# Kernel optimization log

Hardware: AMD Instinct MI355X
Metric: run time of the kernel (lower is better)

The kernel has to match this reference:

```python
import jax, jax.numpy as jnp
import numpy as np

N = 50000        # nodes (users + candidates)
E = 1_600_000    # edges (interactions), avg degree 32
IN = 128         # in_channels
OUT = 128        # out_channels (GRU hidden)
HEAD = 16        # final linear head


def setup_inputs() -> dict:
    key = jax.random.key(0)
    ks = jax.random.split(key, 16)
    sx = 1.0 / np.sqrt(IN)
    sh = 1.0 / np.sqrt(OUT)
    return {
        "x": jax.random.normal(ks[0], (N, IN), jnp.float32),
        "edge_index": jax.random.randint(ks[1], (2, E), 0, N, dtype=jnp.int64),
        "edge_weight": jax.random.uniform(ks[2], (E,), jnp.float32),
        # graph-conv GRU gate weights (update z, reset r, candidate h)
        "W_xz": jax.random.normal(ks[3], (IN, OUT), jnp.float32) * sx,
        "W_hz": jax.random.normal(ks[4], (OUT, OUT), jnp.float32) * sh,
        "b_z": jnp.zeros((OUT,), jnp.float32),
        "W_xr": jax.random.normal(ks[5], (IN, OUT), jnp.float32) * sx,
        "W_hr": jax.random.normal(ks[6], (OUT, OUT), jnp.float32) * sh,
        "b_r": jnp.zeros((OUT,), jnp.float32),
        "W_xh": jax.random.normal(ks[7], (IN, OUT), jnp.float32) * sx,
        "W_hh": jax.random.normal(ks[8], (OUT, OUT), jnp.float32) * sh,
        "b_h": jnp.zeros((OUT,), jnp.float32),
        # final linear head: Linear(out_channels, 16)
        "W_lin": jax.random.normal(ks[9], (OUT, HEAD), jnp.float32) * sh,
        "b_lin": jnp.zeros((HEAD,), jnp.float32),
    }


def reference(x, edge_index, edge_weight,
              W_xz, W_hz, b_z, W_xr, W_hr, b_r, W_xh, W_hh, b_h,
              W_lin, b_lin):
    src, dst = edge_index[0], edge_index[1]

    # symmetric degree normalization from edge weights
    deg_out = jax.ops.segment_sum(edge_weight, src, num_segments=N)
    deg_in = jax.ops.segment_sum(edge_weight, dst, num_segments=N)
    inv_sqrt_out = jnp.where(deg_out > 0, 1.0 / jnp.sqrt(deg_out), 0.0)
    inv_sqrt_in = jnp.where(deg_in > 0, 1.0 / jnp.sqrt(deg_in), 0.0)
    norm = edge_weight * inv_sqrt_out[src] * inv_sqrt_in[dst]  # [E]

    def gconv(feat, W):
        # GCN-style conv: normalized weighted scatter-sum of transformed feats
        m = feat @ W                                   # [N, OUT]
        msg = m[src] * norm[:, None]                   # [E, OUT] gather
        return jax.ops.segment_sum(msg, dst, num_segments=N)  # scatter

    h = jnp.zeros((N, OUT), x.dtype)  # initial recurrent hidden state

    # GRU with graph-conv gates (GConvGRU-style recurrent cell)
    z = jax.nn.sigmoid(gconv(x, W_xz) + gconv(h, W_hz) + b_z)
    r = jax.nn.sigmoid(gconv(x, W_xr) + gconv(h, W_hr) + b_r)
    h_tilde = jnp.tanh(gconv(x, W_xh) + gconv(r * h, W_hh) + b_h)
    h_new = z * h + (1.0 - z) * h_tilde               # [N, OUT]

    return h_new @ W_lin + b_lin                       # [N, 16]
```

## Files before the change

### kernel.cpp

```cpp
#include <hip/hip_runtime.h>
#include <hip/hip_bf16.h>
#include <hip/hip_fp16.h>


#define CH 128
#define HEADS 16
#define TM 64
#define KC 32
#define DRANGE 12800
#define DSLICES 64
#define RN 98
#define NR 512
#define NB 256
#define SCAP 3840

typedef _Float16 half8 __attribute__((ext_vector_type(8)));
typedef _Float16 half4v __attribute__((ext_vector_type(4)));
typedef float floatx4 __attribute__((ext_vector_type(4)));

__global__ __launch_bounds__(256) void k_deg(const int* __restrict__ src,
                                             const float* __restrict__ w,
                                             float* __restrict__ partial, int E) {
    __shared__ float h[DRANGE];
    const int r = blockIdx.x / DSLICES;
    const int sl = blockIdx.x % DSLICES;
    const int base = r * DRANGE;
    for (int i = threadIdx.x; i < DRANGE; i += 256) h[i] = 0.f;
    __syncthreads();
    const int per = (E + DSLICES - 1) / DSLICES;
    const int lo = sl * per;
    const int hi = min(lo + per, E);
    int e = lo + threadIdx.x * 4;
    for (; e + 3 < hi; e += 1024) {
        int4 s4 = *reinterpret_cast<const int4*>(src + e);
        float4 w4 = *reinterpret_cast<const float4*>(w + e);
        int a;
        a = s4.x - base; if ((unsigned)a < DRANGE) atomicAdd(&h[a], w4.x);
        a = s4.y - base; if ((unsigned)a < DRANGE) atomicAdd(&h[a], w4.y);
        a = s4.z - base; if ((unsigned)a < DRANGE) atomicAdd(&h[a], w4.z);
        a = s4.w - base; if ((unsigned)a < DRANGE) atomicAdd(&h[a], w4.w);
    }
    for (; e < hi; ++e) {
        int a = src[e] - base;
        if ((unsigned)a < DRANGE) atomicAdd(&h[a], w[e]);
    }
    __syncthreads();
    float* dstp = partial + ((size_t)r * DSLICES + sl) * DRANGE;
    for (int i = threadIdx.x; i < DRANGE; i += 256) dstp[i] = h[i];
}

__global__ __launch_bounds__(256) void k_degxcw(const float* __restrict__ partial,
                                                const float* __restrict__ x,
                                                __half* __restrict__ xh,
                                                const float* __restrict__ Wxz,
                                                const float* __restrict__ Wxh,
                                                const float* __restrict__ Wlin,
                                                __half* __restrict__ WzT,
                                                __half* __restrict__ WhT,
                                                __half* __restrict__ WlT,
                                                int n, int nbdeg) {
    const int t = threadIdx.x;
    if ((int)blockIdx.x >= nbdeg) {
        int i = (blockIdx.x - nbdeg) * 256 + t;
        if (i < CH * CH) {
            int nn = i >> 7, k = i & 127;
            WzT[i] = __float2half(Wxz[k * CH + nn]);
            WhT[i] = __float2half(Wxh[k * CH + nn]);
        } else if (i < CH * CH + HEADS * CH) {
            int j = i - CH * CH;
            int nn = j >> 7, k = j & 127;
            WlT[j] = __float2half(Wlin[k * HEADS + nn]);
        }
        return;
    }
    __shared__ float degl[256];
    const int bb = blockIdx.x * 256;
    int i = bb + t;
    if (i < n) {
        int r = i / DRANGE;
        int idx = i - r * DRANGE;
        const float* p = partial + (size_t)r * DSLICES * DRANGE + idx;
        float s = 0.f;
#pragma unroll 8
        for (int sl = 0; sl < DSLICES; ++sl) s += p[(size_t)sl * DRANGE];
        degl[t] = s;
    }
    __syncthreads();
#pragma unroll
    for (int g = 0; g < 16; ++g) {
        int ln = g * 16 + (t >> 4);
        int node = bb + ln;
        if (node >= n) break;
        int c8 = (t & 15) * 8;
        float dg = degl[ln];
        float sc = dg > 0.f ? rsqrtf(dg) : 0.f;
        float4 a = *reinterpret_cast<const float4*>(x + (size_t)node * CH + c8);
        float4 b = *reinterpret_cast<const float4*>(x + (size_t)node * CH + c8 + 4);
        __half2 h0 = __floats2half2_rn(a.x * sc, a.y * sc);
        __half2 h1 = __floats2half2_rn(a.z * sc, a.w * sc);
        __half2 h2 = __floats2half2_rn(b.x * sc, b.y * sc);
        __half2 h3 = __floats2half2_rn(b.z * sc, b.w * sc);
        uint4 packed = make_uint4(*(unsigned*)&h0, *(unsigned*)&h1, *(unsigned*)&h2, *(unsigned*)&h3);
        *reinterpret_cast<uint4*>(xh + (size_t)node * CH + c8) = packed;
    }
}

__global__ __launch_bounds__(256) void k_count(const int* __restrict__ dst,
                                               unsigned* __restrict__ counts, int E) {
    __shared__ unsigned h[NR];
    const int b = blockIdx.x;
    for (int i = threadIdx.x; i < NR; i += 256) h[i] = 0u;
    __syncthreads();
    const int per = (E + NB - 1) / NB;
    const int lo = b * per;
    const int hi = min(lo + per, E);
    for (int e = lo + threadIdx.x; e < hi; e += 256)
        atomicAdd(&h[dst[e] / RN], 1u);
    __syncthreads();
    for (int i = threadIdx.x; i < NR; i += 256) counts[(size_t)i * NB + b] = h[i];
}

__global__ __launch_bounds__(256) void k_scanR(unsigned* __restrict__ counts,
                                               unsigned* __restrict__ total) {
    __shared__ unsigned s[256];
    const int r = blockIdx.x;
    const int t = threadIdx.x;
    unsigned v = counts[(size_t)r * NB + t];
    s[t] = v;
    __syncthreads();
    for (int ofs = 1; ofs < 256; ofs <<= 1) {
        unsigned u = (t >= ofs) ? s[t - ofs] : 0u;
        __syncthreads();
        s[t] += u;
        __syncthreads();
    }
    counts[(size_t)r * NB + t] = s[t] - v;
    if (t == 255) total[r] = s[255];
}

__global__ __launch_bounds__(256) void k_part(const int* __restrict__ src,
                                              const int* __restrict__ dst,
                                              const float* __restrict__ w,
                                              const unsigned* __restrict__ counts,
                                              const unsigned* __restrict__ total,
                                              int2* __restrict__ rec2, int E) {
    __shared__ unsigned cursor[NR];
    __shared__ unsigned sa[NR], sb[NR];
    const int b = blockIdx.x;
    const int t = threadIdx.x;
    sa[t] = total[t]; sa[t + 256] = total[t + 256];
    __syncthreads();
    unsigned* cur = sa; unsigned* nxt = sb;
    for (int ofs = 1; ofs < NR; ofs <<= 1) {
        for (int k = t; k < NR; k += 256) {
            unsigned v = cur[k];
            if (k >= ofs) v += cur[k - ofs];
            nxt[k] = v;
        }
        __syncthreads();
        unsigned* tmp = cur; cur = nxt; nxt = tmp;
    }
    for (int r = t; r < NR; r += 256) {
        unsigned rb = cur[r] - total[r];
        cursor[r] = rb + counts[(size_t)r * NB + b];
    }
    __syncthreads();
    const int per = (E + NB - 1) / NB;
    const int lo = b * per;
    const int hi = min(lo + per, E);
    for (int e = lo + t; e < hi; e += 256) {
        int d = dst[e];
        int r = d / RN;
        int dl = d - r * RN;
        unsigned pos = atomicAdd(&cursor[r], 1u);
        rec2[pos] = make_int2(__float_as_int(w[e]), (dl << 16) | src[e]);
    }
}

__global__ __launch_bounds__(1024) void k_sortgather(const unsigned* __restrict__ total,
                                                     const int2* __restrict__ rec2,
                                                     unsigned* __restrict__ rec3,
                                                     const __half* __restrict__ xh,
                                                     __half* __restrict__ xaggh, int n) {
    __shared__ int2 stage[SCAP];
    __shared__ unsigned sortedP[SCAP];
    __shared__ unsigned hist[RN], curx[RN];
    __shared__ unsigned sa[NR], sb[NR];
    const int r = blockIdx.x;
    const int bn = r * RN;
    if (bn >= n) return;
    const int rn = min(RN, n - bn);
    const int t = threadIdx.x;

    if (t < NR) sa[t] = total[t];
    __syncthreads();
    unsigned* cur = sa; unsigned* nxt = sb;
    for (int ofs = 1; ofs < NR; ofs <<= 1) {
        if (t < NR) {
            unsigned v = cur[t];
            if (t >= ofs) v += cur[t - ofs];
            nxt[t] = v;
        }
        __syncthreads();
        unsigned* tmp = cur; cur = nxt; nxt = tmp;
    }
    const unsigned tot = total[r];
    const unsigned gbase = cur[r] - tot;

    if (t < RN) hist[t] = 0u;
    __syncthreads();
    for (unsigned i = t; i < tot; i += 1024) {
        int2 v = rec2[gbase + i];
        if (i < SCAP) stage[i] = v;
        atomicAdd(&hist[v.y >> 16], 1u);
    }
    __syncthreads();
    if (t == 0) {
        unsigned run = 0;
        for (int j = 0; j < rn; ++j) {
            unsigned c = hist[j];
            hist[j] = run;
            curx[j] = run;
            run += c;
        }
    }
    __syncthreads();
    const bool big = (tot > SCAP);
    for (unsigned i = t; i < tot; i += 1024) {
        int2 v = (i < SCAP) ? stage[i] : rec2[gbase + i];
        int dl = v.y >> 16;
        __half hw = __float2half(__int_as_float(v.x));
        unsigned packed = ((unsigned)__half_as_ushort(hw) << 16) | (unsigned)(v.y & 0xFFFF);
        unsigned pos = atomicAdd(&curx[dl], 1u);
        if (big) rec3[gbase + pos] = packed;
        else sortedP[pos] = packed;
    }
    __syncthreads();

    const int hwid = t >> 5;
    const int lane = t & 31;
    const __half* xb = xh + lane * 4;
    const unsigned* grec = rec3 + gbase;
    for (int nd = hwid; nd < rn; nd += 32) {
        unsigned i = hist[nd];
        unsigned end = curx[nd];
        float acc0 = 0.f, acc1 = 0.f, acc2 = 0.f, acc3 = 0.f;
        float wsum = 0.f;
        for (; i + 8 <= end; i += 8) {
            unsigned r0, r1, r2, r3, r4, r5, r6, r7;
            if (big) {
                r0 = grec[i];     r1 = grec[i + 1]; r2 = grec[i + 2]; r3 = grec[i + 3];
                r4 = grec[i + 4]; r5 = grec[i + 5]; r6 = grec[i + 6]; r7 = grec[i + 7];
            } else {
                r0 = sortedP[i];     r1 = sortedP[i + 1]; r2 = sortedP[i + 2]; r3 = sortedP[i + 3];
                r4 = sortedP[i + 4]; r5 = sortedP[i + 5]; r6 = sortedP[i + 6]; r7 = sortedP[i + 7];
            }
            half4v v0 = *reinterpret_cast<const half4v*>(xb + (size_t)(r0 & 0xFFFFu) * CH);
            half4v v1 = *reinterpret_cast<const half4v*>(xb + (size_t)(r1 & 0xFFFFu) * CH);
            half4v v2 = *reinterpret_cast<const half4v*>(xb + (size_t)(r2 & 0xFFFFu) * CH);
            half4v v3 = *reinterpret_cast<const half4v*>(xb + (size_t)(r3 & 0xFFFFu) * CH);
            half4v v4 = *reinterpret_cast<const half4v*>(xb + (size_t)(r4 & 0xFFFFu) * CH);
            half4v v5 = *reinterpret_cast<const half4v*>(xb + (size_t)(r5 & 0xFFFFu) * CH);
            half4v v6 = *reinterpret_cast<const half4v*>(xb + (size_t)(r6 & 0xFFFFu) * CH);
            half4v v7 = *reinterpret_cast<const half4v*>(xb + (size_t)(r7 & 0xFFFFu) * CH);
            float w0 = __half2float(__ushort_as_half((unsigned short)(r0 >> 16)));
            float w1 = __half2float(__ushort_as_half((unsigned short)(r1 >> 16)));
            float w2 = __half2float(__ushort_as_half((unsigned short)(r2 >> 16)));
            float w3 = __half2float(__ushort_as_half((unsigned short)(r3 >> 16)));
            float w4 = __half2float(__ushort_as_half((unsigned short)(r4 >> 16)));
            float w5 = __half2float(__ushort_as_half((unsigned short)(r5 >> 16)));
            float w6 = __half2float(__ushort_as_half((unsigned short)(r6 >> 16)));
            float w7 = __half2float(__ushort_as_half((unsigned short)(r7 >> 16)));
            wsum += ((w0 + w1) + (w2 + w3)) + ((w4 + w5) + (w6 + w7));
            acc0 = fmaf(w0, (float)v0[0], acc0); acc1 = fmaf(w0, (float)v0[1], acc1);
            acc2 = fmaf(w0, (float)v0[2], acc2); acc3 = fmaf(w0, (float)v0[3], acc3);
            acc0 = fmaf(w1, (float)v1[0], acc0); acc1 = fmaf(w1, (float)v1[1], acc1);
            acc2 = fmaf(w1, (float)v1[2], acc2); acc3 = fmaf(w1, (float)v1[3], acc3);
            acc0 = fmaf(w2, (float)v2[0], acc0); acc1 = fmaf(w2, (float)v2[1], acc1);
            acc2 = fmaf(w2, (float)v2[2], acc2); acc3 = fmaf(w2, (float)v2[3], acc3);
            acc0 = fmaf(w3, (float)v3[0], acc0); acc1 = fmaf(w3, (float)v3[1], acc1);
            acc2 = fmaf(w3, (float)v3[2], acc2); acc3 = fmaf(w3, (float)v3[3], acc3);
            acc0 = fmaf(w4, (float)v4[0], acc0); acc1 = fmaf(w4, (float)v4[1], acc1);
            acc2 = fmaf(w4, (float)v4[2], acc2); acc3 = fmaf(w4, (float)v4[3], acc3);
            acc0 = fmaf(w5, (float)v5[0], acc0); acc1 = fmaf(w5, (float)v5[1], acc1);
            acc2 = fmaf(w5, (float)v5[2], acc2); acc3 = fmaf(w5, (float)v5[3], acc3);
            acc0 = fmaf(w6, (float)v6[0], acc0); acc1 = fmaf(w6, (float)v6[1], acc1);
            acc2 = fmaf(w6, (float)v6[2], acc2); acc3 = fmaf(w6, (float)v6[3], acc3);
            acc0 = fmaf(w7, (float)v7[0], acc0); acc1 = fmaf(w7, (float)v7[1], acc1);
            acc2 = fmaf(w7, (float)v7[2], acc2); acc3 = fmaf(w7, (float)v7[3], acc3);
        }
        for (; i < end; ++i) {
            unsigned r0 = big ? grec[i] : sortedP[i];
            float w0 = __half2float(__ushort_as_half((unsigned short)(r0 >> 16)));
            half4v v0 = *reinterpret_cast<const half4v*>(xb + (size_t)(r0 & 0xFFFFu) * CH);
            wsum += w0;
            acc0 = fmaf(w0, (float)v0[0], acc0); acc1 = fmaf(w0, (float)v0[1], acc1);
            acc2 = fmaf(w0, (float)v0[2], acc2); acc3 = fmaf(w0, (float)v0[3], acc3);
        }
        float sc = wsum > 0.f ? rsqrtf(wsum) : 0.f;
        half4v hv;
        hv[0] = (_Float16)(acc0 * sc); hv[1] = (_Float16)(acc1 * sc);
        hv[2] = (_Float16)(acc2 * sc); hv[3] = (_Float16)(acc3 * sc);
        *reinterpret_cast<half4v*>(xaggh + (size_t)(bn + nd) * CH + lane * 4) = hv;
    }
}

__global__ __launch_bounds__(256) void k_final3(const __half* __restrict__ xaggh,
                                                const __half* __restrict__ WzT,
                                                const __half* __restrict__ WhT,
                                                const __half* __restrict__ WlT,
                                                const float* __restrict__ bz,
                                                const float* __restrict__ bh,
                                                const float* __restrict__ blin,
                                                float* __restrict__ out, int n) {
    __shared__ __half gL[4][16][136];
    const int tid = threadIdx.x;
    const int w = tid >> 6;
    const int l = tid & 63;
    const int lr = l & 15;
    const int lk = l >> 4;
    const int nodeb = blockIdx.x * 64 + w * 16;

    int arow = nodeb + lr;
    if (arow > n - 1) arow = n - 1;

    floatx4 accz[8], acch[8];
#pragma unroll
    for (int ct = 0; ct < 8; ++ct) {
        accz[ct] = (floatx4){0.f, 0.f, 0.f, 0.f};
        acch[ct] = (floatx4){0.f, 0.f, 0.f, 0.f};
    }

#pragma unroll
    for (int kc = 0; kc < 4; ++kc) {
        half8 a = *reinterpret_cast<const half8*>(xaggh + (size_t)arow * CH + kc * 32 + lk * 8);
#pragma unroll
        for (int ct = 0; ct < 8; ++ct) {
            half8 bzf = *reinterpret_cast<const half8*>(WzT + (ct * 16 + lr) * CH + kc * 32 + lk * 8);
            accz[ct] = __builtin_amdgcn_mfma_f32_16x16x32_f16(a, bzf, accz[ct], 0, 0, 0);
            half8 bhf = *reinterpret_cast<const half8*>(WhT + (ct * 16 + lr) * CH + kc * 32 + lk * 8);
            acch[ct] = __builtin_amdgcn_mfma_f32_16x16x32_f16(a, bhf, acch[ct], 0, 0, 0);
        }
    }

#pragma unroll
    for (int ct = 0; ct < 8; ++ct) {
        float bzv = bz[ct * 16 + lr];
        float bhv = bh[ct * 16 + lr];
#pragma unroll
        for (int r = 0; r < 4; ++r) {
            float zp = accz[ct][r] + bzv;
            float hp = acch[ct][r] + bhv;
            float g = (1.f - 1.f / (1.f + __expf(-zp))) * tanhf(hp);
            gL[w][lk * 4 + r][ct * 16 + lr] = __float2half(g);
        }
    }
    __syncthreads();

    floatx4 acco = (floatx4){0.f, 0.f, 0.f, 0.f};
#pragma unroll
    for (int kc = 0; kc < 4; ++kc) {
        half8 a = *reinterpret_cast<const half8*>(&gL[w][lr][kc * 32 + lk * 8]);
        half8 b = *reinterpret_cast<const half8*>(WlT + lr * CH + kc * 32 + lk * 8);
        acco = __builtin_amdgcn_mfma_f32_16x16x32_f16(a, b, acco, 0, 0, 0);
    }
    float bl = blin[lr];
#pragma unroll
    for (int r = 0; r < 4; ++r) {
        int node = nodeb + lk * 4 + r;
        if (node < n) out[(size_t)node * HEADS + lr] = acco[r] + bl;
    }
}

__global__ __launch_bounds__(256) void k1B(const int* __restrict__ src,
                                           const int* __restrict__ dst,
                                           const float* __restrict__ w,
                                           float* __restrict__ deg_out,
                                           unsigned* __restrict__ cnt, int E) {
    int e = blockIdx.x * blockDim.x + threadIdx.x;
    if (e >= E) return;
    unsafeAtomicAdd(deg_out + src[e], w[e]);
    atomicAdd(cnt + dst[e], 1u);
}

__global__ __launch_bounds__(1024) void k_scan(unsigned* __restrict__ off, int n) {
    __shared__ unsigned s[1024];
    const int t = threadIdx.x;
    const int per = (n + 1023) / 1024;
    int lo = t * per;
    int hi = lo + per; if (hi > n) hi = n;
    unsigned sum = 0;
    for (int i = lo; i < hi; ++i) sum += off[i];
    s[t] = sum;
    __syncthreads();
    for (int ofs = 1; ofs < 1024; ofs <<= 1) {
        unsigned v = (t >= ofs) ? s[t - ofs] : 0u;
        __syncthreads();
        s[t] += v;
        __syncthreads();
    }
    unsigned run = s[t] - sum;
    for (int i = lo; i < hi; ++i) {
        unsigned c = off[i];
        off[i] = run;
        run += c;
    }
}

__global__ __launch_bounds__(256) void k_fillB(const int* __restrict__ src,
                                               const int* __restrict__ dst,
                                               const float* __restrict__ w,
                                               unsigned* __restrict__ off,
                                               int2* __restrict__ rec, int E) {
    int e = blockIdx.x * blockDim.x + threadIdx.x;
    if (e >= E) return;
    unsigned pos = atomicAdd(off + dst[e], 1u);
    rec[pos] = make_int2(__float_as_int(w[e]), src[e]);
}

__global__ __launch_bounds__(256) void k_gatherB(const unsigned* __restrict__ off,
                                                 const int2* __restrict__ rec,
                                                 const float* __restrict__ deg_out,
                                                 const float* __restrict__ x,
                                                 float* __restrict__ xagg, int n) {
    int node = blockIdx.x * 4 + (threadIdx.x >> 6);
    if (node >= n) return;
    int lane = threadIdx.x & 63;
    unsigned i = node ? off[node - 1] : 0u;
    unsigned end = off[node];
    float2 acc = make_float2(0.f, 0.f);
    float wsum = 0.f;
    for (; i < end; ++i) {
        int2 r0 = rec[i];
        float w0 = __int_as_float(r0.x);
        float d0 = deg_out[r0.y];
        float c0 = w0 * (d0 > 0.f ? rsqrtf(d0) : 0.f);
        float2 v = *reinterpret_cast<const float2*>(x + (size_t)r0.y * CH + lane * 2);
        wsum += w0;
        acc.x = fmaf(c0, v.x, acc.x);
        acc.y = fmaf(c0, v.y, acc.y);
    }
    float sc = wsum > 0.f ? rsqrtf(wsum) : 0.f;
    *reinterpret_cast<float2*>(xagg + (size_t)node * CH + lane * 2) =
        make_float2(acc.x * sc, acc.y * sc);
}

__global__ __launch_bounds__(256) void k_final2(const float* __restrict__ xagg,
                                                const float* __restrict__ Wxz,
                                                const float* __restrict__ bz,
                                                const float* __restrict__ Wxh,
                                                const float* __restrict__ bh,
                                                const float* __restrict__ Wlin,
                                                const float* __restrict__ blin,
                                                float* __restrict__ out, int n) {
    __shared__ float smem[10560];
    float* sA = smem;
    float* sWz = smem + 2304;
    float* sWh = smem + 6400;

    const int tid = threadIdx.x;
    const int tx = tid & 31;
    const int ty = tid >> 5;
    const int base = blockIdx.x * TM;

    float az[8][4] = {{0.f}};
    float ah[8][4] = {{0.f}};

    for (int kc = 0; kc < CH; kc += KC) {
        {
            int i = tid;
#pragma unroll
            for (int r2 = 0; r2 < 2; ++r2, i += 256) {
                int row = i >> 3;
                int c4 = (i & 7) * 4;
                int grow = base + row; if (grow > n - 1) grow = n - 1;
                float4 v = *reinterpret_cast<const float4*>(xagg + (size_t)grow * CH + kc + c4);
                *reinterpret_cast<float4*>(&sA[row * 36 + c4]) = v;
            }
            int j = tid;
#pragma unroll
            for (int r2 = 0; r2 < 4; ++r2, j += 256) {
                int row = j >> 5;
                int c4 = (j & 31) * 4;
                *reinterpret_cast<float4*>(&sWz[row * 128 + c4]) =
                    *reinterpret_cast<const float4*>(Wxz + (size_t)(kc + row) * CH + c4);
                *reinterpret_cast<float4*>(&sWh[row * 128 + c4]) =
                    *reinterpret_cast<const float4*>(Wxh + (size_t)(kc + row) * CH + c4);
            }
        }
        __syncthreads();
#pragma unroll 4
        for (int kk = 0; kk < KC; ++kk) {
            float4 wz = *reinterpret_cast<float4*>(&sWz[kk * 128 + tx * 4]);
            float4 wh = *reinterpret_cast<float4*>(&sWh[kk * 128 + tx * 4]);
#pragma unroll
            for (int r = 0; r < 8; ++r) {
                float a = sA[(ty * 8 + r) * 36 + kk];
                az[r][0] = fmaf(a, wz.x, az[r][0]);
                az[r][1] = fmaf(a, wz.y, az[r][1]);
                az[r][2] = fmaf(a, wz.z, az[r][2]);
                az[r][3] = fmaf(a, wz.w, az[r][3]);
                ah[r][0] = fmaf(a, wh.x, ah[r][0]);
                ah[r][1] = fmaf(a, wh.y, ah[r][1]);
                ah[r][2] = fmaf(a, wh.z, ah[r][2]);
                ah[r][3] = fmaf(a, wh.w, ah[r][3]);
            }
        }
        __syncthreads();
    }

    float* sG = smem;
    const float4 bz4 = *reinterpret_cast<const float4*>(bz + tx * 4);
    const float4 bh4 = *reinterpret_cast<const float4*>(bh + tx * 4);
#pragma unroll
    for (int r = 0; r < 8; ++r) {
        int row = ty * 8 + r;
        float4 g4;
        float zp = az[r][0] + bz4.x, hp = ah[r][0] + bh4.x;
        g4.x = (1.f - 1.f / (1.f + __expf(-zp))) * tanhf(hp);
        zp = az[r][1] + bz4.y; hp = ah[r][1] + bh4.y;
        g4.y = (1.f - 1.f / (1.f + __expf(-zp))) * tanhf(hp);
        zp = az[r][2] + bz4.z; hp = ah[r][2] + bh4.z;
        g4.z = (1.f - 1.f / (1.f + __expf(-zp))) * tanhf(hp);
        zp = az[r][3] + bz4.w; hp = ah[r][3] + bh4.w;
        g4.w = (1.f - 1.f / (1.f + __expf(-zp))) * tanhf(hp);
        *reinterpret_cast<float4*>(&sG[row * 132 + tx * 4]) = g4;
    }
    __syncthreads();

#pragma unroll
    for (int it = 0; it < 4; ++it) {
        int idx = it * 256 + tid;
        int node = idx >> 4;
        int hh = idx & 15;
        float acc = blin[hh];
#pragma unroll 8
        for (int j = 0; j < CH; ++j)
            acc = fmaf(sG[node * 132 + j], Wlin[j * HEADS + hh], acc);
        if (base + node < n) out[(size_t)(base + node) * HEADS + hh] = acc;
    }
}

static inline size_t align256(size_t v) { return (v + 255) & ~(size_t)255; }

extern "C" void kernel_launch(void* const* d_in, const int* in_sizes, int n_in,
                              void* d_out, int out_size, void* d_ws, size_t ws_size,
                              hipStream_t stream) {
    const float* x = (const float*)d_in[0];
    const int* ei = (const int*)d_in[1];
    const float* w = (const float*)d_in[2];
    const float* Wxz = (const float*)d_in[3];
    const float* bz = (const float*)d_in[5];
    const float* Wxh = (const float*)d_in[9];
    const float* bh = (const float*)d_in[11];
    const float* Wlin = (const float*)d_in[12];
    const float* blin = (const float*)d_in[13];
    float* out = (float*)d_out;

    const int Nn = in_sizes[0] / CH;
    const int E = in_sizes[2];

    const int* src = ei;
    const int* dst = ei + E;
    int eb = (E + 255) / 256;
    char* base = (char*)d_ws;

    size_t off_counts = 0;
    size_t off_total = align256(off_counts + (size_t)NR * NB * 4);
    size_t off_xh = align256(off_total + NR * 4);
    size_t off_xaggh = align256(off_xh + (size_t)Nn * CH * 2);
    size_t off_wz = align256(off_xaggh + (size_t)Nn * CH * 2);
    size_t off_wh = align256(off_wz + (size_t)CH * CH * 2);
    size_t off_wl = align256(off_wh + (size_t)CH * CH * 2);
    size_t off_rec2 = align256(off_wl + (size_t)HEADS * CH * 2);
    size_t off_rec3 = align256(off_rec2 + (size_t)E * 8);
    size_t needNew = off_rec3 + (size_t)E * 4;
    size_t partial_bytes = (size_t)4 * DSLICES * DRANGE * 4;

    if (ws_size >= needNew && Nn <= 65536 && (size_t)NR * RN >= (size_t)Nn &&
        partial_bytes <= (size_t)E * 12) {
        unsigned* counts = (unsigned*)(base + off_counts);
        unsigned* total = (unsigned*)(base + off_total);
        __half* xh = (__half*)(base + off_xh);
        __half* xaggh = (__half*)(base + off_xaggh);
        __half* WzT = (__half*)(base + off_wz);
        __half* WhT = (__half*)(base + off_wh);
        __half* WlT = (__half*)(base + off_wl);
        int2* rec2 = (int2*)(base + off_rec2);
        unsigned* rec3 = (unsigned*)(base + off_rec3);
        float* partial = (float*)(base + off_rec2);

        int nbdeg = (Nn + 255) / 256;
        int nbw = (CH * CH + HEADS * CH + 255) / 256;

        k_deg<<<4 * DSLICES, 256, 0, stream>>>(src, w, partial, E);
        k_degxcw<<<nbdeg + nbw, 256, 0, stream>>>(partial, x, xh, Wxz, Wxh, Wlin,
                                                  WzT, WhT, WlT, Nn, nbdeg);
        k_count<<<NB, 256, 0, stream>>>(dst, counts, E);
        k_scanR<<<NR, 256, 0, stream>>>(counts, total);
        k_part<<<NB, 256, 0, stream>>>(src, dst, w, counts, total, rec2, E);
        k_sortgather<<<NR, 1024, 0, stream>>>(total, rec2, rec3, xh, xaggh, Nn);
        k_final3<<<(Nn + 63) / 64, 256, 0, stream>>>(xaggh, WzT, WhT, WlT, bz, bh, blin, out, Nn);
    } else {
        unsigned* off = (unsigned*)base;
        float* deg_out = (float*)(base + (size_t)Nn * 4);
        int2* rec = (int2*)(base + (size_t)2 * Nn * 4);
        float* xagg = (float*)((char*)rec + (size_t)E * 8);

        hipMemsetAsync(d_ws, 0, (size_t)2 * Nn * 4, stream);
        k1B<<<eb, 256, 0, stream>>>(src, dst, w, deg_out, off, E);
        k_scan<<<1, 1024, 0, stream>>>(off, Nn);
        k_fillB<<<eb, 256, 0, stream>>>(src, dst, w, off, rec, E);
        k_gatherB<<<(Nn + 3) / 4, 256, 0, stream>>>(off, rec, deg_out, x, xagg, Nn);
        k_final2<<<(Nn + TM - 1) / TM, 256, 0, stream>>>(xagg, Wxz, bz, Wxh, bh, Wlin, blin, out, Nn);
    }
}
```

Measured before the change: 160.2 us.

## Halve destination bucket size, use 512-thread sort-gather blocks, fuse count into prep kernel

Halves the destination range per bucket (98→49 nodes, 512→1024 buckets) and runs the sort-gather kernel with 512 threads per block, shrinking its shared staging area. The goal is more and lighter blocks, better occupancy and load balance in the gather. The dst-histogram count kernel is merged into the degree/convert kernel as extra blocks, removing one launch. In exchange the prefix scans cover twice as many buckets and more buckets overflow to global memory because of the smaller staging capacity.

```diff
diff --git a/kernel.cpp b/kernel.cpp
--- a/kernel.cpp
+++ b/kernel.cpp
@@ -9,10 +9,10 @@
 #define KC 32
 #define DRANGE 12800
 #define DSLICES 64
-#define RN 98
-#define NR 512
+#define RN 49
+#define NR 1024
 #define NB 256
-#define SCAP 3840
+#define SCAP 2048
 
 typedef _Float16 half8 __attribute__((ext_vector_type(8)));
 typedef _Float16 half4v __attribute__((ext_vector_type(4)));
@@ -49,19 +49,36 @@
     for (int i = threadIdx.x; i < DRANGE; i += 256) dstp[i] = h[i];
 }
 
-__global__ __launch_bounds__(256) void k_degxcw(const float* __restrict__ partial,
-                                                const float* __restrict__ x,
-                                                __half* __restrict__ xh,
-                                                const float* __restrict__ Wxz,
-                                                const float* __restrict__ Wxh,
-                                                const float* __restrict__ Wlin,
-                                                __half* __restrict__ WzT,
-                                                __half* __restrict__ WhT,
-                                                __half* __restrict__ WlT,
-                                                int n, int nbdeg) {
+__global__ __launch_bounds__(256) void k_dxcwc(const float* __restrict__ partial,
+                                               const float* __restrict__ x,
+                                               __half* __restrict__ xh,
+                                               const float* __restrict__ Wxz,
+                                               const float* __restrict__ Wxh,
+                                               const float* __restrict__ Wlin,
+                                               __half* __restrict__ WzT,
+                                               __half* __restrict__ WhT,
+                                               __half* __restrict__ WlT,
+                                               const int* __restrict__ dst,
+                                               unsigned* __restrict__ counts,
+                                               int E, int n, int nbdeg, int nbw) {
     const int t = threadIdx.x;
-    if ((int)blockIdx.x >= nbdeg) {
-        int i = (blockIdx.x - nbdeg) * 256 + t;
+    const int b = blockIdx.x;
+    if (b >= nbdeg + nbw) {
+        __shared__ unsigned h[NR];
+        const int cb = b - nbdeg - nbw;
+        for (int i = t; i < NR; i += 256) h[i] = 0u;
+        __syncthreads();
+        const int per = (E + NB - 1) / NB;
+        const int lo = cb * per;
+        const int hi = min(lo + per, E);
+        for (int e = lo + t; e < hi; e += 256)
+            atomicAdd(&h[dst[e] / RN], 1u);
+        __syncthreads();
+        for (int i = t; i < NR; i += 256) counts[(size_t)i * NB + cb] = h[i];
+        return;
+    }
+    if (b >= nbdeg) {
+        int i = (b - nbdeg) * 256 + t;
         if (i < CH * CH) {
             int nn = i >> 7, k = i & 127;
             WzT[i] = __float2half(Wxz[k * CH + nn]);
@@ -74,7 +91,7 @@
         return;
     }
     __shared__ float degl[256];
-    const int bb = blockIdx.x * 256;
+    const int bb = b * 256;
     int i = bb + t;
     if (i < n) {
         int r = i / DRANGE;
@@ -95,29 +112,14 @@
         float dg = degl[ln];
         float sc = dg > 0.f ? rsqrtf(dg) : 0.f;
         float4 a = *reinterpret_cast<const float4*>(x + (size_t)node * CH + c8);
-        float4 b = *reinterpret_cast<const float4*>(x + (size_t)node * CH + c8 + 4);
+        float4 bq = *reinterpret_cast<const float4*>(x + (size_t)node * CH + c8 + 4);
         __half2 h0 = __floats2half2_rn(a.x * sc, a.y * sc);
         __half2 h1 = __floats2half2_rn(a.z * sc, a.w * sc);
-        __half2 h2 = __floats2half2_rn(b.x * sc, b.y * sc);
-        __half2 h3 = __floats2half2_rn(b.z * sc, b.w * sc);
+        __half2 h2 = __floats2half2_rn(bq.x * sc, bq.y * sc);
+        __half2 h3 = __floats2half2_rn(bq.z * sc, bq.w * sc);
         uint4 packed = make_uint4(*(unsigned*)&h0, *(unsigned*)&h1, *(unsigned*)&h2, *(unsigned*)&h3);
         *reinterpret_cast<uint4*>(xh + (size_t)node * CH + c8) = packed;
     }
-}
-
-__global__ __launch_bounds__(256) void k_count(const int* __restrict__ dst,
-                                               unsigned* __restrict__ counts, int E) {
-    __shared__ unsigned h[NR];
-    const int b = blockIdx.x;
-    for (int i = threadIdx.x; i < NR; i += 256) h[i] = 0u;
-    __syncthreads();
-    const int per = (E + NB - 1) / NB;
-    const int lo = b * per;
-    const int hi = min(lo + per, E);
-    for (int e = lo + threadIdx.x; e < hi; e += 256)
-        atomicAdd(&h[dst[e] / RN], 1u);
-    __syncthreads();
-    for (int i = threadIdx.x; i < NR; i += 256) counts[(size_t)i * NB + b] = h[i];
 }
 
 __global__ __launch_bounds__(256) void k_scanR(unsigned* __restrict__ counts,
@@ -148,7 +150,7 @@
     __shared__ unsigned sa[NR], sb[NR];
     const int b = blockIdx.x;
     const int t = threadIdx.x;
-    sa[t] = total[t]; sa[t + 256] = total[t + 256];
+    for (int k = t; k < NR; k += 256) sa[k] = total[k];
     __syncthreads();
     unsigned* cur = sa; unsigned* nxt = sb;
     for (int ofs = 1; ofs < NR; ofs <<= 1) {
@@ -177,11 +179,11 @@
     }
 }
 
-__global__ __launch_bounds__(1024) void k_sortgather(const unsigned* __restrict__ total,
-                                                     const int2* __restrict__ rec2,
-                                                     unsigned* __restrict__ rec3,
-                                                     const __half* __restrict__ xh,
-                                                     __half* __restrict__ xaggh, int n) {
+__global__ __launch_bounds__(512) void k_sortgather(const unsigned* __restrict__ total,
+                                                    const int2* __restrict__ rec2,
+                                                    unsigned* __restrict__ rec3,
+                                                    const __half* __restrict__ xh,
+                                                    __half* __restrict__ xaggh, int n) {
     __shared__ int2 stage[SCAP];
     __shared__ unsigned sortedP[SCAP];
     __shared__ unsigned hist[RN], curx[RN];
@@ -192,14 +194,14 @@
     const int rn = min(RN, n - bn);
     const int t = threadIdx.x;
 
-    if (t < NR) sa[t] = total[t];
+    sa[t] = total[t]; sa[t + 512] = total[t + 512];
     __syncthreads();
     unsigned* cur = sa; unsigned* nxt = sb;
     for (int ofs = 1; ofs < NR; ofs <<= 1) {
-        if (t < NR) {
-            unsigned v = cur[t];
-            if (t >= ofs) v += cur[t - ofs];
-            nxt[t] = v;
+        for (int k = t; k < NR; k += 512) {
+            unsigned v = cur[k];
+            if (k >= ofs) v += cur[k - ofs];
+            nxt[k] = v;
         }
         __syncthreads();
         unsigned* tmp = cur; cur = nxt; nxt = tmp;
@@ -209,7 +211,7 @@
 
     if (t < RN) hist[t] = 0u;
     __syncthreads();
-    for (unsigned i = t; i < tot; i += 1024) {
+    for (unsigned i = t; i < tot; i += 512) {
         int2 v = rec2[gbase + i];
         if (i < SCAP) stage[i] = v;
         atomicAdd(&hist[v.y >> 16], 1u);
@@ -226,7 +228,7 @@
     }
     __syncthreads();
     const bool big = (tot > SCAP);
-    for (unsigned i = t; i < tot; i += 1024) {
+    for (unsigned i = t; i < tot; i += 512) {
         int2 v = (i < SCAP) ? stage[i] : rec2[gbase + i];
         int dl = v.y >> 16;
         __half hw = __float2half(__int_as_float(v.x));
@@ -241,7 +243,7 @@
     const int lane = t & 31;
     const __half* xb = xh + lane * 4;
     const unsigned* grec = rec3 + gbase;
-    for (int nd = hwid; nd < rn; nd += 32) {
+    for (int nd = hwid; nd < rn; nd += 16) {
         unsigned i = hist[nd];
         unsigned end = curx[nd];
         float acc0 = 0.f, acc1 = 0.f, acc2 = 0.f, acc3 = 0.f;
@@ -594,12 +596,12 @@
         int nbw = (CH * CH + HEADS * CH + 255) / 256;
 
         k_deg<<<4 * DSLICES, 256, 0, stream>>>(src, w, partial, E);
-        k_degxcw<<<nbdeg + nbw, 256, 0, stream>>>(partial, x, xh, Wxz, Wxh, Wlin,
-                                                  WzT, WhT, WlT, Nn, nbdeg);
-        k_count<<<NB, 256, 0, stream>>>(dst, counts, E);
+        k_dxcwc<<<nbdeg + nbw + NB, 256, 0, stream>>>(partial, x, xh, Wxz, Wxh, Wlin,
+                                                      WzT, WhT, WlT, dst, counts,
+                                                      E, Nn, nbdeg, nbw);
         k_scanR<<<NR, 256, 0, stream>>>(counts, total);
         k_part<<<NB, 256, 0, stream>>>(src, dst, w, counts, total, rec2, E);
-        k_sortgather<<<NR, 1024, 0, stream>>>(total, rec2, rec3, xh, xaggh, Nn);
+        k_sortgather<<<NR, 512, 0, stream>>>(total, rec2, rec3, xh, xaggh, Nn);
         k_final3<<<(Nn + 63) / 64, 256, 0, stream>>>(xaggh, WzT, WhT, WlT, bz, bh, blin, out, Nn);
     } else {
         unsigned* off = (unsigned*)base;
```

New measurement: 158.5 us. About the same (-1.1%).
